# Kernel optimization log

Hardware: AMD Instinct MI355X
Metric: run time of the kernel (lower is better)

The kernel has to match this reference:

```python
import jax, jax.numpy as jnp
import numpy as np

# Model config (matches init_kwargs)
B, S = 4, 1024          # batch of equal-length prefill sequences (cu_seqlens = arange(B+1)*S)
H, KVH, D = 16, 4, 64   # query heads, kv heads (GQA), head_dim
SCALE = 0.125           # 1/sqrt(head_dim)
NUM_SLOTS = 8192        # paged-KV-cache total slots


def setup_inputs() -> dict:
    key = jax.random.key(0)
    k1, k2, k3 = jax.random.split(key, 3)
    N = B * S
    q = jax.random.normal(k1, (N, H * D), dtype=jnp.float32)
    k = jax.random.normal(k2, (N, KVH * D), dtype=jnp.float32)
    v = jax.random.normal(k3, (N, KVH * D), dtype=jnp.float32)
    k_cache = jnp.zeros((NUM_SLOTS, KVH * D), dtype=jnp.float32)
    v_cache = jnp.zeros((NUM_SLOTS, KVH * D), dtype=jnp.float32)
    slot_mapping = jnp.arange(N, dtype=jnp.int32)  # valid slots, no -1 entries
    return {"q": q, "k": k, "v": v, "k_cache": k_cache, "v_cache": v_cache,
            "slot_mapping": slot_mapping}


def _varlen_causal_attn(q, k, v):
    # q: [N, H*D], k/v: [N, KVH*D]; equal-length varlen batch -> [B, S, ...]
    qh = q.reshape(B, S, H, D)
    kh = k.reshape(B, S, KVH, D)
    vh = v.reshape(B, S, KVH, D)
    rep = H // KVH  # GQA: repeat kv heads to match query heads
    kh = jnp.repeat(kh, rep, axis=2)
    vh = jnp.repeat(vh, rep, axis=2)
    scores = jnp.einsum('bqhd,bkhd->bhqk', qh, kh) * SCALE
    causal = jnp.tril(jnp.ones((S, S), dtype=bool))
    scores = jnp.where(causal, scores, jnp.finfo(scores.dtype).min)
    p = jax.nn.softmax(scores, axis=-1)
    o = jnp.einsum('bhqk,bkhd->bqhd', p, vh)
    return o.reshape(B * S, H * D)


def reference(q, k, v, k_cache, v_cache, slot_mapping):
    # store_kvcache: scatter new k/v rows into the paged caches (Triton kernel equivalent)
    k_cache = k_cache.at[slot_mapping].set(k)
    v_cache = v_cache.at[slot_mapping].set(v)
    # prefill path: flash_attn_varlen_func(q, k, v, causal=True) on the fresh k/v
    o = _varlen_causal_attn(q, k, v)
    return o, k_cache, v_cache
```

## Files before the change

kernel.cpp:

```cpp
#include <hip/hip_runtime.h>
#include <hip/hip_bf16.h>

#define B_     4
#define S_     1024
#define H_     16
#define KVH_   4
#define D_     64
#define N_     (B_*S_)
#define SLOTS_ 8192
#define KVD_   (KVH_*D_)
#define HD_    (H_*D_)
#define SCL    (0.125f * 1.44269504f)

typedef __attribute__((ext_vector_type(8))) short bf16x8;
typedef __attribute__((ext_vector_type(4))) short bf16x4;
typedef __attribute__((ext_vector_type(4))) float f32x4;

__device__ __forceinline__ short4 f4tob4(float4 f){
    union { __hip_bfloat162 h[2]; short4 s; } u;
    u.h[0] = __float22bfloat162_rn(make_float2(f.x, f.y));
    u.h[1] = __float22bfloat162_rn(make_float2(f.z, f.w));
    return u.s;
}
__device__ __forceinline__ int swz(int row, int col){
    return row*64 + (col ^ ((row & 7) << 3));
}

__global__ __launch_bounds__(256) void copy_caches(
    const float4* __restrict__ kcin, const float4* __restrict__ vcin,
    float4* __restrict__ kc, float4* __restrict__ vc){
    int i = blockIdx.x*256 + threadIdx.x;
    kc[i] = kcin[i];
    vc[i] = vcin[i];
}

__global__ __launch_bounds__(256) void prep_kernel(
    const float* __restrict__ k, const float* __restrict__ v,
    const int* __restrict__ slot_map,
    float* __restrict__ kc, float* __restrict__ vc,
    short* __restrict__ Kb, short* __restrict__ Vtb)
{
    __shared__ short sv[64*68];
    const int tid = threadIdx.x;
    const int g   = blockIdx.x >> 4;
    const int s0  = (blockIdx.x & 15) * 64;
    const int b   = g >> 2, kvh = g & 3;

    const int sl = tid >> 2;
    const int cq = (tid & 3) * 16;

    const int n   = b*S_ + s0 + sl;
    const int pos = s0 + sl;
    const float4* kp = (const float4*)(k + (size_t)n*KVD_ + kvh*D_ + cq);
    const float4* vp = (const float4*)(v + (size_t)n*KVD_ + kvh*D_ + cq);
    const int s = slot_map[n];

    float4 kk[4], vv[4];
    #pragma unroll
    for (int j = 0; j < 4; ++j){ kk[j] = kp[j]; vv[j] = vp[j]; }

    if (s >= 0){
        float4* kcp = (float4*)(kc + (size_t)s*KVD_ + kvh*D_ + cq);
        float4* vcp = (float4*)(vc + (size_t)s*KVD_ + kvh*D_ + cq);
        #pragma unroll
        for (int j = 0; j < 4; ++j){ kcp[j] = kk[j]; vcp[j] = vv[j]; }
    }

    short* kbp = Kb + ((size_t)g*S_ + pos)*64 + cq;
    #pragma unroll
    for (int j = 0; j < 4; ++j)
        *(short4*)(kbp + j*4) = f4tob4(kk[j]);

    #pragma unroll
    for (int j = 0; j < 4; ++j)
        *(short4*)(&sv[sl*68 + cq + j*4]) = f4tob4(vv[j]);
    __syncthreads();

    const int d  = tid >> 2;
    const int sg = (tid & 3) * 16;
    union { short s[16]; bf16x8 v8[2]; } out;
    #pragma unroll
    for (int i = 0; i < 16; ++i)
        out.s[i] = sv[(sg + i)*68 + d];
    short* vtp = Vtb + ((size_t)g*64 + d)*S_ + s0 + sg;
    *(bf16x8*)(vtp)     = out.v8[0];
    *(bf16x8*)(vtp + 8) = out.v8[1];
}

__global__ __launch_bounds__(256, 2) void attn_kernel(
    const float* __restrict__ q, const short* __restrict__ Kb,
    const short* __restrict__ Vtb, float* __restrict__ o)
{
    __shared__ __align__(16) short sK[2][64*64];
    __shared__ __align__(16) short sV[2][64*64];

    const int tid  = threadIdx.x;
    const int wave = tid >> 6;
    const int lane = tid & 63;
    const int quad = lane >> 4;
    const int l16  = lane & 15;

    const int bid = blockIdx.x;
    const int g   = bid & 15;
    const int p   = bid >> 4;
    const int qtA = p, qtB = 63 - p;
    const int ntA = (qtA >> 2) + 1;
    const int ntB = (qtB >> 2) + 1;

    const int b = g >> 2, kvh = g & 3;
    const int h = kvh*4 + wave;

    bf16x8 qfA[2], qfB[2];
    {
        const float* qpA = q + ((size_t)(b*S_ + qtA*16 + l16))*HD_ + h*D_ + quad*8;
        const float* qpB = q + ((size_t)(b*S_ + qtB*16 + l16))*HD_ + h*D_ + quad*8;
        #pragma unroll
        for (int ks = 0; ks < 2; ++ks){
            float4 a0 = *(const float4*)(qpA + ks*32);
            float4 a1 = *(const float4*)(qpA + ks*32 + 4);
            float4 b0 = *(const float4*)(qpB + ks*32);
            float4 b1 = *(const float4*)(qpB + ks*32 + 4);
            a0.x*=SCL; a0.y*=SCL; a0.z*=SCL; a0.w*=SCL;
            a1.x*=SCL; a1.y*=SCL; a1.z*=SCL; a1.w*=SCL;
            b0.x*=SCL; b0.y*=SCL; b0.z*=SCL; b0.w*=SCL;
            b1.x*=SCL; b1.y*=SCL; b1.z*=SCL; b1.w*=SCL;
            union { short4 s[2]; bf16x8 v8; } ua, ub;
            ua.s[0] = f4tob4(a0); ua.s[1] = f4tob4(a1);
            ub.s[0] = f4tob4(b0); ub.s[1] = f4tob4(b1);
            qfA[ks] = ua.v8; qfB[ks] = ub.v8;
        }
    }

    f32x4 ofA[4], ofB[4];
    #pragma unroll
    for (int f2 = 0; f2 < 4; ++f2){
        ofA[f2] = (f32x4){0.f,0.f,0.f,0.f};
        ofB[f2] = (f32x4){0.f,0.f,0.f,0.f};
    }
    float lsA = 0.f, lsB = 0.f;
    const int qrowA = qtA*16 + l16, qrowB = qtB*16 + l16;

    const short* Kg = Kb  + (size_t)g*S_*64;
    const short* Vg = Vtb + (size_t)g*64*S_;

    const int rs = tid >> 2;
    const int cg = (tid & 3) * 16;

    bf16x8 kst[2], vst[2];
    kst[0] = *(const bf16x8*)(Kg + (size_t)rs*64 + cg);
    kst[1] = *(const bf16x8*)(Kg + (size_t)rs*64 + cg + 8);
    vst[0] = *(const bf16x8*)(Vg + (size_t)rs*S_ + cg);
    vst[1] = *(const bf16x8*)(Vg + (size_t)rs*S_ + cg + 8);

    auto pv_body = [&](const f32x4* sc, f32x4* of, float& lsum,
                       int qrow, bool diag, int t, const short* V_){
        bf16x4 pfrag[4];
        #pragma unroll
        for (int f = 0; f < 4; ++f){
            float4 pf;
            #pragma unroll
            for (int r = 0; r < 4; ++r){
                float pe = __builtin_amdgcn_exp2f(sc[f][r]);
                if (diag && (t*64 + f*16 + quad*4 + r > qrow)) pe = 0.f;
                lsum += pe;
                ((float*)&pf)[r] = pe;
            }
            union { short4 s; bf16x4 bv; } u; u.s = f4tob4(pf);
            pfrag[f] = u.bv;
        }
        #pragma unroll
        for (int f = 0; f < 4; ++f){
            #pragma unroll
            for (int f2 = 0; f2 < 4; ++f2){
                bf16x4 vf = *(const bf16x4*)(&V_[swz(f2*16 + l16, f*16 + quad*4)]);
                of[f2] = __builtin_amdgcn_mfma_f32_16x16x16bf16_1k(pfrag[f], vf, of[f2], 0, 0, 0);
            }
        }
    };

    for (int t = 0; t < ntB; ++t){
        short* K_ = (short*)sK[t & 1];
        short* V_ = (short*)sV[t & 1];
        *(bf16x8*)(&K_[swz(rs, cg)])     = kst[0];
        *(bf16x8*)(&K_[swz(rs, cg + 8)]) = kst[1];
        *(bf16x8*)(&V_[swz(rs, cg)])     = vst[0];
        *(bf16x8*)(&V_[swz(rs, cg + 8)]) = vst[1];
        if (t + 1 < ntB){
            kst[0] = *(const bf16x8*)(Kg + (size_t)((t+1)*64 + rs)*64 + cg);
            kst[1] = *(const bf16x8*)(Kg + (size_t)((t+1)*64 + rs)*64 + cg + 8);
            vst[0] = *(const bf16x8*)(Vg + (size_t)rs*S_ + (t+1)*64 + cg);
            vst[1] = *(const bf16x8*)(Vg + (size_t)rs*S_ + (t+1)*64 + cg + 8);
        }
        __syncthreads();

        bf16x8 kf[2][4];
        #pragma unroll
        for (int ks = 0; ks < 2; ++ks)
            #pragma unroll
            for (int f = 0; f < 4; ++f)
                kf[ks][f] = *(const bf16x8*)(&K_[swz(f*16 + l16, ks*32 + quad*8)]);

        const bool actA = (t < ntA);

        f32x4 scB[4];
        #pragma unroll
        for (int f = 0; f < 4; ++f) scB[f] = (f32x4){0.f,0.f,0.f,0.f};
        #pragma unroll
        for (int ks = 0; ks < 2; ++ks)
            #pragma unroll
            for (int f = 0; f < 4; ++f)
                scB[f] = __builtin_amdgcn_mfma_f32_16x16x32_bf16(kf[ks][f], qfB[ks], scB[f], 0, 0, 0);
        pv_body(scB, ofB, lsB, qrowB, t == ntB - 1, t, V_);

        if (actA){
            f32x4 scA[4];
            #pragma unroll
            for (int f = 0; f < 4; ++f) scA[f] = (f32x4){0.f,0.f,0.f,0.f};
            #pragma unroll
            for (int ks = 0; ks < 2; ++ks)
                #pragma unroll
                for (int f = 0; f < 4; ++f)
                    scA[f] = __builtin_amdgcn_mfma_f32_16x16x32_bf16(kf[ks][f], qfA[ks], scA[f], 0, 0, 0);
            pv_body(scA, ofA, lsA, qrowA, t == ntA - 1, t, V_);
        }
    }

    auto epilogue = [&](f32x4* of, float lsum, int qt){
        lsum += __shfl_xor(lsum, 16);
        lsum += __shfl_xor(lsum, 32);
        float linv[4];
        #pragma unroll
        for (int r = 0; r < 4; ++r)
            linv[r] = 1.f / __shfl(lsum, quad*4 + r);
        #pragma unroll
        for (int f2 = 0; f2 < 4; ++f2){
            #pragma unroll
            for (int r = 0; r < 4; ++r){
                const int row = qt*16 + quad*4 + r;
                o[((size_t)(b*S_ + row))*HD_ + h*D_ + f2*16 + l16] = of[f2][r] * linv[r];
            }
        }
    };
    epilogue(ofA, lsA, qtA);
    epilogue(ofB, lsB, qtB);
}

extern "C" void kernel_launch(void* const* d_in, const int* in_sizes, int n_in,
                              void* d_out, int out_size, void* d_ws, size_t ws_size,
                              hipStream_t stream){
    (void)in_sizes; (void)n_in; (void)out_size; (void)ws_size;
    const float* q     = (const float*)d_in[0];
    const float* k     = (const float*)d_in[1];
    const float* v     = (const float*)d_in[2];
    const float* kc_in = (const float*)d_in[3];
    const float* vc_in = (const float*)d_in[4];
    const int*   slot  = (const int*)d_in[5];

    float* o  = (float*)d_out;
    float* kc = o + (size_t)N_*HD_;
    float* vc = kc + (size_t)SLOTS_*KVD_;

    short* Kb = (short*)d_ws;
    short* Vt = Kb + (size_t)16*S_*64;

    copy_caches<<<(SLOTS_*64)/256, 256, 0, stream>>>(
        (const float4*)kc_in, (const float4*)vc_in, (float4*)kc, (float4*)vc);

    prep_kernel<<<256, 256, 0, stream>>>(k, v, slot, kc, vc, Kb, Vt);

    attn_kernel<<<512, 256, 0, stream>>>(q, Kb, Vt, o);
}
```

Baseline: 119.0 us.

## Merge cache copy into prep kernel and move slot scatter into attention kernel

Folds the full cache copy into the prep kernel as extra blocks, so copy and K/V bf16 conversion run in one launch instead of two. The slot-mapped scatter of k/v into the caches moves into the prologue of the attention kernel, where each block writes 8 rows before its attention work. This saves a launch and lets the scatter overlap with attention. In exchange the attention kernel carries extra global traffic and registers. Correctness relies on stream ordering, since the copy in the prep launch must finish before the scatter overwrites the caches.

```diff
diff --git a/kernel.cpp b/kernel.cpp
--- a/kernel.cpp
+++ b/kernel.cpp
@@ -26,22 +26,25 @@
     return row*64 + (col ^ ((row & 7) << 3));
 }
 
-__global__ __launch_bounds__(256) void copy_caches(
+__global__ __launch_bounds__(256) void prep_copy(
+    const float* __restrict__ k, const float* __restrict__ v,
     const float4* __restrict__ kcin, const float4* __restrict__ vcin,
-    float4* __restrict__ kc, float4* __restrict__ vc){
-    int i = blockIdx.x*256 + threadIdx.x;
-    kc[i] = kcin[i];
-    vc[i] = vcin[i];
-}
-
-__global__ __launch_bounds__(256) void prep_kernel(
-    const float* __restrict__ k, const float* __restrict__ v,
-    const int* __restrict__ slot_map,
-    float* __restrict__ kc, float* __restrict__ vc,
+    float4* __restrict__ kc4, float4* __restrict__ vc4,
     short* __restrict__ Kb, short* __restrict__ Vtb)
 {
     __shared__ short sv[64*68];
     const int tid = threadIdx.x;
+
+    if (blockIdx.x >= 256){
+        const int base = (blockIdx.x - 256)*1024 + tid;
+        #pragma unroll
+        for (int j = 0; j < 4; ++j){
+            kc4[base + j*256] = kcin[base + j*256];
+            vc4[base + j*256] = vcin[base + j*256];
+        }
+        return;
+    }
+
     const int g   = blockIdx.x >> 4;
     const int s0  = (blockIdx.x & 15) * 64;
     const int b   = g >> 2, kvh = g & 3;
@@ -53,18 +56,10 @@
     const int pos = s0 + sl;
     const float4* kp = (const float4*)(k + (size_t)n*KVD_ + kvh*D_ + cq);
     const float4* vp = (const float4*)(v + (size_t)n*KVD_ + kvh*D_ + cq);
-    const int s = slot_map[n];
 
     float4 kk[4], vv[4];
     #pragma unroll
     for (int j = 0; j < 4; ++j){ kk[j] = kp[j]; vv[j] = vp[j]; }
-
-    if (s >= 0){
-        float4* kcp = (float4*)(kc + (size_t)s*KVD_ + kvh*D_ + cq);
-        float4* vcp = (float4*)(vc + (size_t)s*KVD_ + kvh*D_ + cq);
-        #pragma unroll
-        for (int j = 0; j < 4; ++j){ kcp[j] = kk[j]; vcp[j] = vv[j]; }
-    }
 
     short* kbp = Kb + ((size_t)g*S_ + pos)*64 + cq;
     #pragma unroll
@@ -89,7 +84,10 @@
 
 __global__ __launch_bounds__(256, 2) void attn_kernel(
     const float* __restrict__ q, const short* __restrict__ Kb,
-    const short* __restrict__ Vtb, float* __restrict__ o)
+    const short* __restrict__ Vtb, float* __restrict__ o,
+    const float* __restrict__ k, const float* __restrict__ v,
+    const int* __restrict__ slot_map,
+    float* __restrict__ kc, float* __restrict__ vc)
 {
     __shared__ __align__(16) short sK[2][64*64];
     __shared__ __align__(16) short sV[2][64*64];
@@ -101,6 +99,21 @@
     const int l16  = lane & 15;
 
     const int bid = blockIdx.x;
+
+    {
+        const int n = bid*8 + (tid >> 5);
+        const int c = (tid & 31) * 8;
+        const float4* kp = (const float4*)(k + (size_t)n*KVD_ + c);
+        const float4* vp = (const float4*)(v + (size_t)n*KVD_ + c);
+        float4 a0 = kp[0], a1 = kp[1], b0 = vp[0], b1 = vp[1];
+        const int s = slot_map[n];
+        if (s >= 0){
+            float4* kcp = (float4*)(kc + (size_t)s*KVD_ + c);
+            float4* vcp = (float4*)(vc + (size_t)s*KVD_ + c);
+            kcp[0] = a0; kcp[1] = a1; vcp[0] = b0; vcp[1] = b1;
+        }
+    }
+
     const int g   = bid & 15;
     const int p   = bid >> 4;
     const int qtA = p, qtB = 63 - p;
@@ -263,10 +276,9 @@
     short* Kb = (short*)d_ws;
     short* Vt = Kb + (size_t)16*S_*64;
 
-    copy_caches<<<(SLOTS_*64)/256, 256, 0, stream>>>(
-        (const float4*)kc_in, (const float4*)vc_in, (float4*)kc, (float4*)vc);
-
-    prep_kernel<<<256, 256, 0, stream>>>(k, v, slot, kc, vc, Kb, Vt);
-
-    attn_kernel<<<512, 256, 0, stream>>>(q, Kb, Vt, o);
-}
+    prep_copy<<<768, 256, 0, stream>>>(
+        k, v, (const float4*)kc_in, (const float4*)vc_in,
+        (float4*)kc, (float4*)vc, Kb, Vt);
+
+    attn_kernel<<<512, 256, 0, stream>>>(q, Kb, Vt, o, k, v, slot, kc, vc);
+}
```

After: 114.4 us. 1.04x faster.
